# Optimization experiments

Hardware: AMD Instinct MI355X
Metric: run time of the kernel (lower is better)

The kernel has to match this reference:

```python
import jax, jax.numpy as jnp
import numpy as np

B, N, L, OUT = 64, 100, 32, 3
EDGE_SIZES = [64, 64]   # edge MLP widths per mp step
NODE_SIZES = [64, 32]   # node MLP widths per mp step
ALPHA = 0.1             # leaky relu slope
NUM_MPS = 2
EPS = 1e-12             # for differentiable euclidean norm


def _lin_init(key, fan_in, fan_out):
    k1, k2 = jax.random.split(key)
    s = 1.0 / np.sqrt(fan_in)
    w = jax.random.uniform(k1, (fan_in, fan_out), jnp.float32, -s, s)
    b = jax.random.uniform(k2, (fan_out,), jnp.float32, -s, s)
    return w, b


def setup_inputs() -> dict:
    key = jax.random.key(0)
    ks = iter(jax.random.split(key, 32))
    inp = {"x": jax.random.normal(next(ks), (B, L), jnp.float32)}
    # global latent map: Linear(L, N*L)
    inp["lin_w"], inp["lin_b"] = _lin_init(next(ks), L, N * L)
    d = L
    for i in range(NUM_MPS):
        e_in = 2 * d + 1  # [x_i, x_j, dist_ij]
        inp[f"e{i}_w0"], inp[f"e{i}_b0"] = _lin_init(next(ks), e_in, EDGE_SIZES[0])
        inp[f"e{i}_w1"], inp[f"e{i}_b1"] = _lin_init(next(ks), EDGE_SIZES[0], EDGE_SIZES[1])
        n_in = d + EDGE_SIZES[1]  # [x, aggregated edges]
        inp[f"n{i}_w0"], inp[f"n{i}_b0"] = _lin_init(next(ks), n_in, NODE_SIZES[0])
        inp[f"n{i}_w1"], inp[f"n{i}_b1"] = _lin_init(next(ks), NODE_SIZES[0], NODE_SIZES[1])
        d = NODE_SIZES[1]
    inp["out_w"], inp["out_b"] = _lin_init(next(ks), d, OUT)
    return inp


def _mlp(h, layers, alpha):
    for w, b in layers:
        h = jax.nn.leaky_relu(h @ w + b, alpha)
    return h


def _forward(x, lin_w, lin_b,
             e0_w0, e0_b0, e0_w1, e0_b1, n0_w0, n0_b0, n0_w1, n0_b1,
             e1_w0, e1_b0, e1_w1, e1_b1, n1_w0, n1_b0, n1_w1, n1_b1,
             out_w, out_b):
    # latent map: [B, L] -> [B, N, L]
    h = (x @ lin_w + lin_b).reshape(-1, N, L)
    steps = [
        ([(e0_w0, e0_b0), (e0_w1, e0_b1)], [(n0_w0, n0_b0), (n0_w1, n0_b1)]),
        ([(e1_w0, e1_b0), (e1_w1, e1_b1)], [(n1_w0, n1_b0), (n1_w1, n1_b1)]),
    ]
    for edge_layers, node_layers in steps:
        b, n, d = h.shape
        xi = h[:, :, None, :]  # [B, N, 1, d] (receiver)
        xj = h[:, None, :, :]  # [B, 1, N, d] (sender)
        # euclidean pairwise distance, eps for differentiability at 0
        dist = jnp.sqrt(jnp.sum((xi - xj) ** 2, axis=-1, keepdims=True) + EPS)
        e_in = jnp.concatenate([
            jnp.broadcast_to(xi, (b, n, n, d)),
            jnp.broadcast_to(xj, (b, n, n, d)),
            dist,
        ], axis=-1)                       # [B, N, N, 2d+1]
        A = _mlp(e_in, edge_layers, ALPHA)  # [B, N, N, e_out]
        agg = A.sum(axis=2)               # sum over senders -> [B, N, e_out]
        h = _mlp(jnp.concatenate([h, agg], axis=-1), node_layers, ALPHA)
    out = h @ out_w + out_b               # [B, N, OUT]
    return jnp.tanh(out)                  # normalize_output=True


def reference(x, lin_w, lin_b,
              e0_w0, e0_b0, e0_w1, e0_b1, n0_w0, n0_b0, n0_w1, n0_b1,
              e1_w0, e1_b0, e1_w1, e1_b1, n1_w0, n1_b0, n1_w1, n1_b1,
              out_w, out_b):
    return _forward(x, lin_w, lin_b,
                    e0_w0, e0_b0, e0_w1, e0_b1, n0_w0, n0_b0, n0_w1, n0_b1,
                    e1_w0, e1_b0, e1_w1, e1_b1, n1_w0, n1_b0, n1_w1, n1_b1,
                    out_w, out_b)
```

## Files before the change

### kernel.cpp

```cpp
#include <hip/hip_runtime.h>

#define NB 64
#define NN 100
#define DL 32
#define BN (NB * NN)

typedef _Float16 f16x8 __attribute__((ext_vector_type(8)));
typedef float f32x4 __attribute__((ext_vector_type(4)));

static __device__ __forceinline__ float lrelu(float x) { return fmaxf(x, 0.1f * x); }
static __device__ __forceinline__ f32x4 ld4(const float* p) { return *(const f32x4*)p; }
static __device__ __forceinline__ float hsum4(f32x4 v) { return v[0] + v[1] + v[2] + v[3]; }

__global__ __launch_bounds__(256) void k_pre(
    const float* __restrict__ x, const float* __restrict__ lw, const float* __restrict__ lb,
    const float* __restrict__ ew0, const float* __restrict__ eb0,
    const float* __restrict__ w1a, const float* __restrict__ w1b,
    float* __restrict__ h, float* __restrict__ U, _Float16* __restrict__ V,
    _Float16* __restrict__ PW) {
    int blk = blockIdx.x;
    int t = threadIdx.x;
    if (blk >= 1600) {
        int step = blk - 1600;
        const float* w1 = step ? w1b : w1a;
        _Float16* dst = PW + step * 4096;
#pragma unroll
        for (int u = 0; u < 16; ++u) {
            int idx = t * 16 + u;
            int jj = idx & 7, lane = (idx >> 3) & 63, hf = (idx >> 9) & 1, kt = idx >> 10;
            int c = hf * 32 + (lane >> 4) * 8 + jj;
            int k = kt * 16 + (lane & 15);
            dst[idx] = (_Float16)w1[c * 64 + k];
        }
        return;
    }
    __shared__ float xs[DL];
    __shared__ float hs[4][DL];
    int row0 = blk * 4;
    int b = row0 / NN;
    if (t < DL) xs[t] = x[b * DL + t];
    __syncthreads();
    if (t < 128) {
        int ni = t >> 5, c = t & 31;
        int n = (row0 + ni) % NN;
        float s = lb[n * DL + c];
#pragma unroll
        for (int cc = 0; cc < DL; ++cc) s += xs[cc] * lw[cc * 3200 + n * DL + c];
        hs[ni][c] = s;
        h[(row0 + ni) * DL + c] = s;
    }
    __syncthreads();
#pragma unroll
    for (int r = 0; r < 2; ++r) {
        int o = r * 256 + t;
        int ni = o >> 7, kw = o & 127;
        int which = kw >> 6, k = kw & 63;
        const float* wp = ew0 + (which ? DL * 64 : 0) + k;
        float s = which ? 0.f : eb0[k];
#pragma unroll
        for (int c = 0; c < DL; ++c) s += hs[ni][c] * wp[c * 64];
        if (which) V[(row0 + ni) * 64 + k] = (_Float16)s;
        else       U[(row0 + ni) * 64 + k] = s;
    }
}

template <int FINAL>
__global__ __launch_bounds__(256) void k_edge(
    const float* __restrict__ h, const float* __restrict__ U, const _Float16* __restrict__ V,
    const float* __restrict__ w0, const _Float16* __restrict__ PW,
    const float* __restrict__ b1,
    const float* __restrict__ w0n, const float* __restrict__ b0n,
    const float* __restrict__ w1n, const float* __restrict__ b1n,
    const float* __restrict__ wA, const float* __restrict__ bA,
    float* __restrict__ hout, float* __restrict__ Uo, _Float16* __restrict__ Vo,
    float* __restrict__ out) {
    __shared__ __align__(16) _Float16 pwl[4096];
    __shared__ float sdist[4][112];
    __shared__ __align__(16) float sxin[4][96];
    __shared__ __align__(16) float st0[4][64];
    __shared__ __align__(16) float sh2[4][32];
    __shared__ __align__(16) float swn0[96 * 64];

    int t = threadIdx.x;
    {
        const f16x8* srcp = (const f16x8*)PW;
        f16x8* dstp = (f16x8*)pwl;
        dstp[t] = srcp[t];
        dstp[t + 256] = srcp[t + 256];
        const f32x4* s0 = (const f32x4*)w0n;
        f32x4* d0 = (f32x4*)swn0;
#pragma unroll
        for (int i = 0; i < 6; ++i) d0[t + i * 256] = s0[t + i * 256];
    }
    int w = t >> 6, lane = t & 63, q = lane >> 4, kk = lane & 15;
    int bi = blockIdx.x * 4 + w;
    int b = bi / NN;

    if (lane < 32) sxin[w][lane] = h[bi * DL + lane];

    {
        int g = lane >> 2, r = lane & 3;
        const float* hi = h + bi * DL + r * 8;
        f32x4 hi0 = ld4(hi), hi1 = ld4(hi + 4);
        const float* hb = h + b * NN * DL;
#pragma unroll
        for (int it = 0; it < 7; ++it) {
            int j = it * 16 + g;
            int jc = j < NN ? j : NN - 1;
            const float* hj = hb + jc * DL + r * 8;
            f32x4 d0 = hi0 - ld4(hj);
            f32x4 d1 = hi1 - ld4(hj + 4);
            f32x4 s4 = d0 * d0 + d1 * d1;
            float s = hsum4(s4);
            s += __shfl_xor(s, 1);
            s += __shfl_xor(s, 2);
            if (r == 0) sdist[w][j] = sqrtf(s + 1e-12f);
        }
    }

    int c0 = q * 8;
    f16x8 ulo, uhi, wdlo, wdhi;
    {
        const float* Up = U + (size_t)bi * 64;
        f32x4 a0 = ld4(Up + c0), a1 = ld4(Up + c0 + 4);
        f32x4 a2 = ld4(Up + 32 + c0), a3 = ld4(Up + 36 + c0);
        const float* wd = w0 + 64 * 64;
        f32x4 d0 = ld4(wd + c0), d1 = ld4(wd + c0 + 4);
        f32x4 d2 = ld4(wd + 32 + c0), d3 = ld4(wd + 36 + c0);
#pragma unroll
        for (int i = 0; i < 4; ++i) {
            ulo[i] = (_Float16)a0[i];  ulo[i + 4] = (_Float16)a1[i];
            uhi[i] = (_Float16)a2[i];  uhi[i + 4] = (_Float16)a3[i];
            wdlo[i] = (_Float16)d0[i]; wdlo[i + 4] = (_Float16)d1[i];
            wdhi[i] = (_Float16)d2[i]; wdhi[i + 4] = (_Float16)d3[i];
        }
    }
    float b1k[4];
#pragma unroll
    for (int kt = 0; kt < 4; ++kt) b1k[kt] = b1[kt * 16 + kk];
    float m6 = (q == 0) ? 1.f : 0.f;

    const _Float16* Vb = V + (size_t)b * NN * 64;
    f16x8 vlo, vhi;
    {
        const _Float16* vr = Vb + kk * 64 + c0;
        vlo = *(const f16x8*)vr;
        vhi = *(const f16x8*)(vr + 32);
    }

    __syncthreads();
    float dj = sdist[w][kk];

    float sacc[4] = {0.f, 0.f, 0.f, 0.f};
    unsigned pb = 0;
#pragma unroll
    for (int jt = 0; jt < 7; ++jt) {
        _Float16 djh = (_Float16)dj;
        f16x8 dj8;
#pragma unroll
        for (int i = 0; i < 8; ++i) dj8[i] = djh;
        f16x8 A0 = __builtin_elementwise_fma(dj8, wdlo, ulo + vlo);
        f16x8 A1 = __builtin_elementwise_fma(dj8, wdhi, uhi + vhi);
        A0 = __builtin_elementwise_max(A0, (_Float16)0.1f * A0);
        A1 = __builtin_elementwise_max(A1, (_Float16)0.1f * A1);

        if (jt < 6) {
            int j = (jt + 1) * 16 + kk;
            int jc = (jt == 5 && j >= NN) ? NN - 1 : j;
            const _Float16* vr = Vb + jc * 64 + c0;
            vlo = *(const f16x8*)vr;
            vhi = *(const f16x8*)(vr + 32);
            dj = sdist[w][j];
        }
        asm volatile("" : "+v"(pb));
        const _Float16* pB = (const _Float16*)((const char*)pwl + pb);
        __builtin_amdgcn_s_setprio(1);
#pragma unroll
        for (int kt = 0; kt < 4; ++kt) {
            f16x8 B0 = *(const f16x8*)&pB[(kt * 2 + 0) * 512 + lane * 8];
            f16x8 B1 = *(const f16x8*)&pB[(kt * 2 + 1) * 512 + lane * 8];
            f32x4 a = {0.f, 0.f, 0.f, 0.f};
            a = __builtin_amdgcn_mfma_f32_16x16x32_f16(A0, B0, a, 0, 0, 0);
            a = __builtin_amdgcn_mfma_f32_16x16x32_f16(A1, B1, a, 0, 0, 0);
            f32x4 s4 = a + b1k[kt];
            s4 = __builtin_elementwise_max(s4, 0.1f * s4);
            float hs = hsum4(s4);
            sacc[kt] += (jt == 6) ? hs * m6 : hs;
        }
        __builtin_amdgcn_s_setprio(0);
    }

    {
        float ag[4];
#pragma unroll
        for (int kt = 0; kt < 4; ++kt) {
            float s = sacc[kt];
            s += __shfl_xor(s, 16);
            s += __shfl_xor(s, 32);
            ag[kt] = s;
        }
        if (lane < 16) {
#pragma unroll
            for (int kt = 0; kt < 4; ++kt) sxin[w][32 + kt * 16 + lane] = ag[kt];
        }
    }

    {
        float sa = 0.f, sb = 0.f, sc = 0.f, sd = 0.f;
#pragma unroll
        for (int c4 = 0; c4 < 24; ++c4) {
            f32x4 xv = ld4(&sxin[w][c4 * 4]);
            sa += xv[0] * swn0[(c4 * 4 + 0) * 64 + lane];
            sb += xv[1] * swn0[(c4 * 4 + 1) * 64 + lane];
            sc += xv[2] * swn0[(c4 * 4 + 2) * 64 + lane];
            sd += xv[3] * swn0[(c4 * 4 + 3) * 64 + lane];
        }
        st0[w][lane] = lrelu((sa + sb) + (sc + sd) + b0n[lane]);
    }
    {
        int k2 = lane & 31, p = lane >> 5;
        float sa = 0.f, sb = 0.f, sc = 0.f, sd = 0.f;
#pragma unroll
        for (int c4 = 0; c4 < 8; ++c4) {
            f32x4 xv = ld4(&st0[w][p * 32 + c4 * 4]);
            int c = p * 32 + c4 * 4;
            sa += xv[0] * w1n[(c + 0) * DL + k2];
            sb += xv[1] * w1n[(c + 1) * DL + k2];
            sc += xv[2] * w1n[(c + 2) * DL + k2];
            sd += xv[3] * w1n[(c + 3) * DL + k2];
        }
        float s = (sa + sb) + (sc + sd);
        s += __shfl_xor(s, 32);
        if (lane < 32) {
            float hv = lrelu(s + b1n[lane]);
            sh2[w][lane] = hv;
            if (!FINAL) hout[bi * DL + lane] = hv;
        }
    }

    if (FINAL) {
        if (lane < 3) {
            float s = bA[lane];
#pragma unroll
            for (int c4 = 0; c4 < 8; ++c4) {
                f32x4 xv = ld4(&sh2[w][c4 * 4]);
#pragma unroll
                for (int i = 0; i < 4; ++i) s += xv[i] * wA[(c4 * 4 + i) * 3 + lane];
            }
            out[bi * 3 + lane] = tanhf(s);
        }
    } else {
        float su = bA[lane], sv = 0.f;
#pragma unroll
        for (int c4 = 0; c4 < 8; ++c4) {
            f32x4 xv = ld4(&sh2[w][c4 * 4]);
#pragma unroll
            for (int i = 0; i < 4; ++i) {
                int c = c4 * 4 + i;
                su += xv[i] * wA[c * 64 + lane];
                sv += xv[i] * wA[(DL + c) * 64 + lane];
            }
        }
        Uo[bi * 64 + lane] = su;
        Vo[bi * 64 + lane] = (_Float16)sv;
    }
}

extern "C" void kernel_launch(void* const* d_in, const int* in_sizes, int n_in,
                              void* d_out, int out_size, void* d_ws, size_t ws_size,
                              hipStream_t stream) {
    const float* x     = (const float*)d_in[0];
    const float* lin_w = (const float*)d_in[1];
    const float* lin_b = (const float*)d_in[2];
    const float* ew0[2] = {(const float*)d_in[3],  (const float*)d_in[11]};
    const float* eb0[2] = {(const float*)d_in[4],  (const float*)d_in[12]};
    const float* ew1[2] = {(const float*)d_in[5],  (const float*)d_in[13]};
    const float* eb1[2] = {(const float*)d_in[6],  (const float*)d_in[14]};
    const float* nw0[2] = {(const float*)d_in[7],  (const float*)d_in[15]};
    const float* nb0[2] = {(const float*)d_in[8],  (const float*)d_in[16]};
    const float* nw1[2] = {(const float*)d_in[9],  (const float*)d_in[17]};
    const float* nb1[2] = {(const float*)d_in[10], (const float*)d_in[18]};
    const float* ow = (const float*)d_in[19];
    const float* ob = (const float*)d_in[20];
    float* out = (float*)d_out;

    float* h    = (float*)d_ws;
    float* h2   = h + 204800;
    float* U    = h2 + 204800;
    float* U2   = U + 409600;
    _Float16* V  = (_Float16*)(U2 + 409600);
    _Float16* V2 = V + 409600;
    _Float16* PW = V2 + 409600;

    k_pre<<<1602, 256, 0, stream>>>(x, lin_w, lin_b, ew0[0], eb0[0], ew1[0], ew1[1],
                                    h, U, V, PW);
    k_edge<0><<<1600, 256, 0, stream>>>(h, U, V, ew0[0], PW, eb1[0],
                                        nw0[0], nb0[0], nw1[0], nb1[0],
                                        ew0[1], eb0[1], h2, U2, V2, nullptr);
    k_edge<1><<<1600, 256, 0, stream>>>(h2, U2, V2, ew0[1], PW + 4096, eb1[1],
                                        nw0[1], nb0[1], nw1[1], nb1[1],
                                        ow, ob, nullptr, nullptr, nullptr, out);
}
```

Before: 158.8 us.

## Process two receiver nodes per wavefront to reuse sender V and weight loads

```diff
diff --git a/kernel.cpp b/kernel.cpp
--- a/kernel.cpp
+++ b/kernel.cpp
@@ -75,10 +75,10 @@
     float* __restrict__ hout, float* __restrict__ Uo, _Float16* __restrict__ Vo,
     float* __restrict__ out) {
     __shared__ __align__(16) _Float16 pwl[4096];
-    __shared__ float sdist[4][112];
-    __shared__ __align__(16) float sxin[4][96];
-    __shared__ __align__(16) float st0[4][64];
-    __shared__ __align__(16) float sh2[4][32];
+    __shared__ float sdist[8][112];
+    __shared__ __align__(16) float sxin[8][96];
+    __shared__ __align__(16) float st0[8][64];
+    __shared__ __align__(16) float sh2[8][32];
     __shared__ __align__(16) float swn0[96 * 64];
 
     int t = threadIdx.x;
@@ -93,47 +93,59 @@
         for (int i = 0; i < 6; ++i) d0[t + i * 256] = s0[t + i * 256];
     }
     int w = t >> 6, lane = t & 63, q = lane >> 4, kk = lane & 15;
-    int bi = blockIdx.x * 4 + w;
-    int b = bi / NN;
-
-    if (lane < 32) sxin[w][lane] = h[bi * DL + lane];
+    int bi0 = blockIdx.x * 8 + w * 2;
+    int b = bi0 / NN;
+
+    {
+        int r2 = lane >> 5, c = lane & 31;
+        sxin[w * 2 + r2][c] = h[(bi0 + r2) * DL + c];
+    }
 
     {
         int g = lane >> 2, r = lane & 3;
-        const float* hi = h + bi * DL + r * 8;
-        f32x4 hi0 = ld4(hi), hi1 = ld4(hi + 4);
         const float* hb = h + b * NN * DL;
 #pragma unroll
-        for (int it = 0; it < 7; ++it) {
-            int j = it * 16 + g;
-            int jc = j < NN ? j : NN - 1;
-            const float* hj = hb + jc * DL + r * 8;
-            f32x4 d0 = hi0 - ld4(hj);
-            f32x4 d1 = hi1 - ld4(hj + 4);
-            f32x4 s4 = d0 * d0 + d1 * d1;
-            float s = hsum4(s4);
-            s += __shfl_xor(s, 1);
-            s += __shfl_xor(s, 2);
-            if (r == 0) sdist[w][j] = sqrtf(s + 1e-12f);
+        for (int r2 = 0; r2 < 2; ++r2) {
+            const float* hi = h + (bi0 + r2) * DL + r * 8;
+            f32x4 hi0 = ld4(hi), hi1 = ld4(hi + 4);
+#pragma unroll
+            for (int it = 0; it < 7; ++it) {
+                int j = it * 16 + g;
+                int jc = j < NN ? j : NN - 1;
+                const float* hj = hb + jc * DL + r * 8;
+                f32x4 d0 = hi0 - ld4(hj);
+                f32x4 d1 = hi1 - ld4(hj + 4);
+                f32x4 s4 = d0 * d0 + d1 * d1;
+                float s = hsum4(s4);
+                s += __shfl_xor(s, 1);
+                s += __shfl_xor(s, 2);
+                if (r == 0) sdist[w * 2 + r2][j] = sqrtf(s + 1e-12f);
+            }
         }
     }
 
     int c0 = q * 8;
-    f16x8 ulo, uhi, wdlo, wdhi;
-    {
-        const float* Up = U + (size_t)bi * 64;
-        f32x4 a0 = ld4(Up + c0), a1 = ld4(Up + c0 + 4);
-        f32x4 a2 = ld4(Up + 32 + c0), a3 = ld4(Up + 36 + c0);
+    f16x8 wdlo, wdhi, ulo[2], uhi[2];
+    {
         const float* wd = w0 + 64 * 64;
         f32x4 d0 = ld4(wd + c0), d1 = ld4(wd + c0 + 4);
         f32x4 d2 = ld4(wd + 32 + c0), d3 = ld4(wd + 36 + c0);
 #pragma unroll
         for (int i = 0; i < 4; ++i) {
-            ulo[i] = (_Float16)a0[i];  ulo[i + 4] = (_Float16)a1[i];
-            uhi[i] = (_Float16)a2[i];  uhi[i + 4] = (_Float16)a3[i];
             wdlo[i] = (_Float16)d0[i]; wdlo[i + 4] = (_Float16)d1[i];
             wdhi[i] = (_Float16)d2[i]; wdhi[i + 4] = (_Float16)d3[i];
         }
+#pragma unroll
+        for (int r2 = 0; r2 < 2; ++r2) {
+            const float* Up = U + (size_t)(bi0 + r2) * 64;
+            f32x4 a0 = ld4(Up + c0), a1 = ld4(Up + c0 + 4);
+            f32x4 a2 = ld4(Up + 32 + c0), a3 = ld4(Up + 36 + c0);
+#pragma unroll
+            for (int i = 0; i < 4; ++i) {
+                ulo[r2][i] = (_Float16)a0[i];  ulo[r2][i + 4] = (_Float16)a1[i];
+                uhi[r2][i] = (_Float16)a2[i];  uhi[r2][i + 4] = (_Float16)a3[i];
+            }
+        }
     }
     float b1k[4];
 #pragma unroll
@@ -141,36 +153,45 @@
     float m6 = (q == 0) ? 1.f : 0.f;
 
     const _Float16* Vb = V + (size_t)b * NN * 64;
-    f16x8 vlo, vhi;
+    f16x8 vlo[2], vhi[2];
     {
         const _Float16* vr = Vb + kk * 64 + c0;
-        vlo = *(const f16x8*)vr;
-        vhi = *(const f16x8*)(vr + 32);
+        vlo[0] = *(const f16x8*)vr;
+        vhi[0] = *(const f16x8*)(vr + 32);
+        vlo[1] = vlo[0];
+        vhi[1] = vhi[0];
     }
 
     __syncthreads();
-    float dj = sdist[w][kk];
-
-    float sacc[4] = {0.f, 0.f, 0.f, 0.f};
+    float dj[2];
+    dj[0] = sdist[w * 2 + 0][kk];
+    dj[1] = sdist[w * 2 + 1][kk];
+
+    float sacc[2][4] = {{0.f, 0.f, 0.f, 0.f}, {0.f, 0.f, 0.f, 0.f}};
     unsigned pb = 0;
 #pragma unroll
     for (int jt = 0; jt < 7; ++jt) {
-        _Float16 djh = (_Float16)dj;
-        f16x8 dj8;
-#pragma unroll
-        for (int i = 0; i < 8; ++i) dj8[i] = djh;
-        f16x8 A0 = __builtin_elementwise_fma(dj8, wdlo, ulo + vlo);
-        f16x8 A1 = __builtin_elementwise_fma(dj8, wdhi, uhi + vhi);
-        A0 = __builtin_elementwise_max(A0, (_Float16)0.1f * A0);
-        A1 = __builtin_elementwise_max(A1, (_Float16)0.1f * A1);
+        f16x8 A0[2], A1[2];
+#pragma unroll
+        for (int r2 = 0; r2 < 2; ++r2) {
+            _Float16 djh = (_Float16)dj[r2];
+            f16x8 dj8;
+#pragma unroll
+            for (int i = 0; i < 8; ++i) dj8[i] = djh;
+            f16x8 a0v = __builtin_elementwise_fma(dj8, wdlo, ulo[r2] + vlo[0]);
+            f16x8 a1v = __builtin_elementwise_fma(dj8, wdhi, uhi[r2] + vhi[0]);
+            A0[r2] = __builtin_elementwise_max(a0v, (_Float16)0.1f * a0v);
+            A1[r2] = __builtin_elementwise_max(a1v, (_Float16)0.1f * a1v);
+        }
 
         if (jt < 6) {
             int j = (jt + 1) * 16 + kk;
             int jc = (jt == 5 && j >= NN) ? NN - 1 : j;
             const _Float16* vr = Vb + jc * 64 + c0;
-            vlo = *(const f16x8*)vr;
-            vhi = *(const f16x8*)(vr + 32);
-            dj = sdist[w][j];
+            vlo[0] = *(const f16x8*)vr;
+            vhi[0] = *(const f16x8*)(vr + 32);
+            dj[0] = sdist[w * 2 + 0][j];
+            dj[1] = sdist[w * 2 + 1][j];
         }
         asm volatile("" : "+v"(pb));
         const _Float16* pB = (const _Float16*)((const char*)pwl + pb);
@@ -179,90 +200,98 @@
         for (int kt = 0; kt < 4; ++kt) {
             f16x8 B0 = *(const f16x8*)&pB[(kt * 2 + 0) * 512 + lane * 8];
             f16x8 B1 = *(const f16x8*)&pB[(kt * 2 + 1) * 512 + lane * 8];
-            f32x4 a = {0.f, 0.f, 0.f, 0.f};
-            a = __builtin_amdgcn_mfma_f32_16x16x32_f16(A0, B0, a, 0, 0, 0);
-            a = __builtin_amdgcn_mfma_f32_16x16x32_f16(A1, B1, a, 0, 0, 0);
-            f32x4 s4 = a + b1k[kt];
-            s4 = __builtin_elementwise_max(s4, 0.1f * s4);
-            float hs = hsum4(s4);
-            sacc[kt] += (jt == 6) ? hs * m6 : hs;
+#pragma unroll
+            for (int r2 = 0; r2 < 2; ++r2) {
+                f32x4 a = {0.f, 0.f, 0.f, 0.f};
+                a = __builtin_amdgcn_mfma_f32_16x16x32_f16(A0[r2], B0, a, 0, 0, 0);
+                a = __builtin_amdgcn_mfma_f32_16x16x32_f16(A1[r2], B1, a, 0, 0, 0);
+                f32x4 s4 = a + b1k[kt];
+                s4 = __builtin_elementwise_max(s4, 0.1f * s4);
+                float hs = hsum4(s4);
+                sacc[r2][kt] += (jt == 6) ? hs * m6 : hs;
+            }
         }
         __builtin_amdgcn_s_setprio(0);
     }
 
-    {
+#pragma unroll
+    for (int r2 = 0; r2 < 2; ++r2) {
         float ag[4];
 #pragma unroll
         for (int kt = 0; kt < 4; ++kt) {
-            float s = sacc[kt];
+            float s = sacc[r2][kt];
             s += __shfl_xor(s, 16);
             s += __shfl_xor(s, 32);
             ag[kt] = s;
         }
         if (lane < 16) {
 #pragma unroll
-            for (int kt = 0; kt < 4; ++kt) sxin[w][32 + kt * 16 + lane] = ag[kt];
-        }
-    }
-
-    {
-        float sa = 0.f, sb = 0.f, sc = 0.f, sd = 0.f;
-#pragma unroll
-        for (int c4 = 0; c4 < 24; ++c4) {
-            f32x4 xv = ld4(&sxin[w][c4 * 4]);
-            sa += xv[0] * swn0[(c4 * 4 + 0) * 64 + lane];
-            sb += xv[1] * swn0[(c4 * 4 + 1) * 64 + lane];
-            sc += xv[2] * swn0[(c4 * 4 + 2) * 64 + lane];
-            sd += xv[3] * swn0[(c4 * 4 + 3) * 64 + lane];
-        }
-        st0[w][lane] = lrelu((sa + sb) + (sc + sd) + b0n[lane]);
-    }
-    {
-        int k2 = lane & 31, p = lane >> 5;
-        float sa = 0.f, sb = 0.f, sc = 0.f, sd = 0.f;
-#pragma unroll
-        for (int c4 = 0; c4 < 8; ++c4) {
-            f32x4 xv = ld4(&st0[w][p * 32 + c4 * 4]);
-            int c = p * 32 + c4 * 4;
-            sa += xv[0] * w1n[(c + 0) * DL + k2];
-            sb += xv[1] * w1n[(c + 1) * DL + k2];
-            sc += xv[2] * w1n[(c + 2) * DL + k2];
-            sd += xv[3] * w1n[(c + 3) * DL + k2];
-        }
-        float s = (sa + sb) + (sc + sd);
-        s += __shfl_xor(s, 32);
-        if (lane < 32) {
-            float hv = lrelu(s + b1n[lane]);
-            sh2[w][lane] = hv;
-            if (!FINAL) hout[bi * DL + lane] = hv;
-        }
-    }
-
-    if (FINAL) {
-        if (lane < 3) {
-            float s = bA[lane];
+            for (int kt = 0; kt < 4; ++kt) sxin[w * 2 + r2][32 + kt * 16 + lane] = ag[kt];
+        }
+    }
+
+#pragma unroll
+    for (int r2 = 0; r2 < 2; ++r2) {
+        int slot = w * 2 + r2;
+        int bi = bi0 + r2;
+        {
+            float sa = 0.f, sb = 0.f, sc = 0.f, sd = 0.f;
+#pragma unroll
+            for (int c4 = 0; c4 < 24; ++c4) {
+                f32x4 xv = ld4(&sxin[slot][c4 * 4]);
+                sa += xv[0] * swn0[(c4 * 4 + 0) * 64 + lane];
+                sb += xv[1] * swn0[(c4 * 4 + 1) * 64 + lane];
+                sc += xv[2] * swn0[(c4 * 4 + 2) * 64 + lane];
+                sd += xv[3] * swn0[(c4 * 4 + 3) * 64 + lane];
+            }
+            st0[slot][lane] = lrelu((sa + sb) + (sc + sd) + b0n[lane]);
+        }
+        {
+            int k2 = lane & 31, p = lane >> 5;
+            float sa = 0.f, sb = 0.f, sc = 0.f, sd = 0.f;
 #pragma unroll
             for (int c4 = 0; c4 < 8; ++c4) {
-                f32x4 xv = ld4(&sh2[w][c4 * 4]);
-#pragma unroll
-                for (int i = 0; i < 4; ++i) s += xv[i] * wA[(c4 * 4 + i) * 3 + lane];
-            }
-            out[bi * 3 + lane] = tanhf(s);
-        }
-    } else {
-        float su = bA[lane], sv = 0.f;
-#pragma unroll
-        for (int c4 = 0; c4 < 8; ++c4) {
-            f32x4 xv = ld4(&sh2[w][c4 * 4]);
-#pragma unroll
-            for (int i = 0; i < 4; ++i) {
-                int c = c4 * 4 + i;
-                su += xv[i] * wA[c * 64 + lane];
-                sv += xv[i] * wA[(DL + c) * 64 + lane];
-            }
-        }
-        Uo[bi * 64 + lane] = su;
-        Vo[bi * 64 + lane] = (_Float16)sv;
+                f32x4 xv = ld4(&st0[slot][p * 32 + c4 * 4]);
+                int c = p * 32 + c4 * 4;
+                sa += xv[0] * w1n[(c + 0) * DL + k2];
+                sb += xv[1] * w1n[(c + 1) * DL + k2];
+                sc += xv[2] * w1n[(c + 2) * DL + k2];
+                sd += xv[3] * w1n[(c + 3) * DL + k2];
+            }
+            float s = (sa + sb) + (sc + sd);
+            s += __shfl_xor(s, 32);
+            if (lane < 32) {
+                float hv = lrelu(s + b1n[lane]);
+                sh2[slot][lane] = hv;
+                if (!FINAL) hout[bi * DL + lane] = hv;
+            }
+        }
+        if (FINAL) {
+            if (lane < 3) {
+                float s = bA[lane];
+#pragma unroll
+                for (int c4 = 0; c4 < 8; ++c4) {
+                    f32x4 xv = ld4(&sh2[slot][c4 * 4]);
+#pragma unroll
+                    for (int i = 0; i < 4; ++i) s += xv[i] * wA[(c4 * 4 + i) * 3 + lane];
+                }
+                out[bi * 3 + lane] = tanhf(s);
+            }
+        } else {
+            float su = bA[lane], sv = 0.f;
+#pragma unroll
+            for (int c4 = 0; c4 < 8; ++c4) {
+                f32x4 xv = ld4(&sh2[slot][c4 * 4]);
+#pragma unroll
+                for (int i = 0; i < 4; ++i) {
+                    int c = c4 * 4 + i;
+                    su += xv[i] * wA[c * 64 + lane];
+                    sv += xv[i] * wA[(DL + c) * 64 + lane];
+                }
+            }
+            Uo[bi * 64 + lane] = su;
+            Vo[bi * 64 + lane] = (_Float16)sv;
+        }
     }
 }
 
@@ -294,10 +323,10 @@
 
     k_pre<<<1602, 256, 0, stream>>>(x, lin_w, lin_b, ew0[0], eb0[0], ew1[0], ew1[1],
                                     h, U, V, PW);
-    k_edge<0><<<1600, 256, 0, stream>>>(h, U, V, ew0[0], PW, eb1[0],
-                                        nw0[0], nb0[0], nw1[0], nb1[0],
-                                        ew0[1], eb0[1], h2, U2, V2, nullptr);
-    k_edge<1><<<1600, 256, 0, stream>>>(h2, U2, V2, ew0[1], PW + 4096, eb1[1],
-                                        nw0[1], nb0[1], nw1[1], nb1[1],
-                                        ow, ob, nullptr, nullptr, nullptr, out);
+    k_edge<0><<<800, 256, 0, stream>>>(h, U, V, ew0[0], PW, eb1[0],
+                                       nw0[0], nb0[0], nw1[0], nb1[0],
+                                       ew0[1], eb0[1], h2, U2, V2, nullptr);
+    k_edge<1><<<800, 256, 0, stream>>>(h2, U2, V2, ew0[1], PW + 4096, eb1[1],
+                                       nw0[1], nb0[1], nw1[1], nb1[1],
+                                       ow, ob, nullptr, nullptr, nullptr, out);
 }
```

Result: slower. 189.8 us (+19.5%).
